# Kernel tuning notes

Measured on AMD Instinct MI355X. Metric: run time of the kernel, lower is better.

The kernel has to match this reference:

```python
import jax, jax.numpy as jnp
import numpy as np

N, K, D, L = 50000, 32, 128, 64
NEG_SLOPE = 0.2


def setup_inputs() -> dict:
    key = jax.random.key(0)
    k1, k2, k3, k4 = jax.random.split(key, 4)
    para_neighbors = jax.random.normal(k1, (N, K, D), dtype=jnp.float32)
    para_nei_labels = jax.random.uniform(k2, (N, K, L), dtype=jnp.float32)
    # glorot-uniform-style params
    lim_lin = float(np.sqrt(6.0 / (D + D)))
    linear = jax.random.uniform(k3, (D, D), minval=-lim_lin, maxval=lim_lin, dtype=jnp.float32)
    lim_e = float(np.sqrt(6.0 / (D + 1)))
    e_vec = jax.random.uniform(k4, (D, 1), minval=-lim_e, maxval=lim_e, dtype=jnp.float32)
    bias = jnp.zeros((K, 1), dtype=jnp.float32)
    return {"para_neighbors": para_neighbors, "para_nei_labels": para_nei_labels,
            "linear": linear, "e_vec": e_vec, "bias": bias}


def reference(para_neighbors, para_nei_labels, linear, e_vec, bias):
    # [N, K, D] @ [D, D] -> [N, K, D], LeakyReLU(0.2)
    h = jax.nn.leaky_relu(jnp.einsum('nkd,de->nke', para_neighbors, linear), NEG_SLOPE)
    # attention logits: [N, K, 1] + bias [K, 1] -> LeakyReLU
    e = jax.nn.leaky_relu(jnp.einsum('nkd,do->nko', h, e_vec) + bias, NEG_SLOPE)
    # softmax over neighbor axis (axis=1)
    alpha = jax.nn.softmax(e, axis=1)[..., 0]  # [N, K]
    # weighted label aggregation: [N, K] x [N, K, L] -> [N, L]
    pred_labels = jnp.einsum('nk,nkl->nl', alpha, para_nei_labels)
    return pred_labels
```

## Files before the change

kernel.cpp:

```cpp
#include <hip/hip_runtime.h>
#include <hip/hip_bf16.h>

#define NN 50000
#define KK 32
#define DD 128
#define LL 64
#define NEG 0.2f

typedef __bf16 bf16x8 __attribute__((ext_vector_type(8)));
typedef unsigned short u16x8 __attribute__((ext_vector_type(8)));
typedef float f32x4 __attribute__((ext_vector_type(4)));

__device__ __forceinline__ unsigned short f2bf(float f) {
    unsigned u = __builtin_bit_cast(unsigned, f);
    unsigned r = (u + 0x7fffu + ((u >> 16) & 1u)) >> 16;
    return (unsigned short)r;
}

__device__ __forceinline__ bf16x8 pack_bf16x8(float4 a, float4 b) {
    bf16x8 t;
    t[0] = (__bf16)a.x; t[1] = (__bf16)a.y; t[2] = (__bf16)a.z; t[3] = (__bf16)a.w;
    t[4] = (__bf16)b.x; t[5] = (__bf16)b.y; t[6] = (__bf16)b.z; t[7] = (__bf16)b.w;
    return t;
}


__global__ void prep_w_kernel(const float* __restrict__ lin,
                              unsigned short* __restrict__ wimg) {
    int idx = blockIdx.x * blockDim.x + threadIdx.x;
    if (idx >= DD * DD) return;
    int d = idx >> 7;
    int e = idx & 127;
    unsigned b = (unsigned)e * 256u + (unsigned)d * 2u;
    b ^= ((unsigned)(e & 7)) << 4;
    wimg[b >> 1] = f2bf(lin[idx]);
}

__global__ __launch_bounds__(256)
void attn_fused_kernel(const float* __restrict__ X,
                       const float* __restrict__ LAB,
                       const unsigned short* __restrict__ WIMG,
                       const float* __restrict__ EV,
                       const float* __restrict__ BIAS,
                       float* __restrict__ OUT)
{
    __shared__ __align__(16) unsigned short w_lds[DD * DD];
    __shared__ float alpha_lds[4 * 64];

    const int tid  = threadIdx.x;
    const int wave = tid >> 6;
    const int lane = tid & 63;
    const int lo16 = lane & 15;
    const int g    = lane >> 4;

    {
        const float4* wsrc = reinterpret_cast<const float4*>(WIMG);
        float4* wdst = reinterpret_cast<float4*>(w_lds);
        #pragma unroll
        for (int i = 0; i < 8; ++i)
            wdst[i * 256 + tid] = wsrc[i * 256 + tid];
    }

    float evr[8];
    #pragma unroll
    for (int ct = 0; ct < 8; ++ct) evr[ct] = EV[ct * 16 + lo16];

    float biasr[2][4];
    #pragma unroll
    for (int h = 0; h < 2; ++h)
        #pragma unroll
        for (int r = 0; r < 4; ++r)
            biasr[h][r] = BIAS[h * 16 + g * 4 + r];

    const long rowbase = (long)blockIdx.x * 256 + wave * 64;
    bf16x8 a[4][4];
    #pragma unroll
    for (int mt = 0; mt < 4; ++mt) {
        const float* xr = X + (rowbase + mt * 16 + lo16) * (long)DD;
        #pragma unroll
        for (int kt = 0; kt < 4; ++kt) {
            const float4* p = reinterpret_cast<const float4*>(xr + kt * 32 + g * 8);
            float4 u0 = p[0];
            float4 u1 = p[1];
            a[mt][kt] = pack_bf16x8(u0, u1);
        }
    }

    __syncthreads();

    float pe[4][4];
    #pragma unroll
    for (int mt = 0; mt < 4; ++mt)
        #pragma unroll
        for (int r = 0; r < 4; ++r) pe[mt][r] = 0.f;

    const char* wl = reinterpret_cast<const char*>(w_lds);
    #pragma unroll
    for (int ct = 0; ct < 8; ++ct) {
        bf16x8 b[4];
        const int n = ct * 16 + lo16;
        #pragma unroll
        for (int kt = 0; kt < 4; ++kt) {
            unsigned off = (unsigned)(n * 256 + kt * 64 + g * 16);
            off ^= ((unsigned)(n & 7)) << 4;
            b[kt] = *reinterpret_cast<const bf16x8*>(wl + off);
        }
        f32x4 acc[4];
        #pragma unroll
        for (int mt = 0; mt < 4; ++mt) { acc[mt][0]=0.f; acc[mt][1]=0.f; acc[mt][2]=0.f; acc[mt][3]=0.f; }
        #pragma unroll
        for (int kt = 0; kt < 4; ++kt)
            #pragma unroll
            for (int mt = 0; mt < 4; ++mt)
                acc[mt] = __builtin_amdgcn_mfma_f32_16x16x32_bf16(a[mt][kt], b[kt], acc[mt], 0, 0, 0);
        #pragma unroll
        for (int mt = 0; mt < 4; ++mt)
            #pragma unroll
            for (int r = 0; r < 4; ++r) {
                float h = acc[mt][r];
                h = (h > 0.f) ? h : NEG * h;
                pe[mt][r] += h * evr[ct];
            }
    }

    #pragma unroll
    for (int mt = 0; mt < 4; ++mt)
        #pragma unroll
        for (int r = 0; r < 4; ++r) {
            float v = pe[mt][r];
            v += __shfl_xor(v, 1);
            v += __shfl_xor(v, 2);
            v += __shfl_xor(v, 4);
            v += __shfl_xor(v, 8);
            v += biasr[mt & 1][r];
            pe[mt][r] = (v > 0.f) ? v : NEG * v;
        }

    #pragma unroll
    for (int h = 0; h < 2; ++h) {
        float m = -3.4e38f;
        #pragma unroll
        for (int t = 0; t < 2; ++t)
            #pragma unroll
            for (int r = 0; r < 4; ++r) m = fmaxf(m, pe[2 * h + t][r]);
        m = fmaxf(m, __shfl_xor(m, 16));
        m = fmaxf(m, __shfl_xor(m, 32));
        float p[2][4];
        float s = 0.f;
        #pragma unroll
        for (int t = 0; t < 2; ++t)
            #pragma unroll
            for (int r = 0; r < 4; ++r) {
                p[t][r] = __expf(pe[2 * h + t][r] - m);
                s += p[t][r];
            }
        s += __shfl_xor(s, 16);
        s += __shfl_xor(s, 32);
        float inv = 1.f / s;
        if (lo16 == 0) {
            #pragma unroll
            for (int t = 0; t < 2; ++t)
                #pragma unroll
                for (int r = 0; r < 4; ++r)
                    alpha_lds[wave * 64 + h * 32 + t * 16 + g * 4 + r] = p[t][r] * inv;
        }
    }

    __syncthreads();

    const int c2 = (lane & 31) * 2;
    const int kh = lane >> 5;
    #pragma unroll
    for (int h = 0; h < 2; ++h) {
        const long n = (long)blockIdx.x * 8 + wave * 2 + h;
        const float* lab = LAB + n * (long)(KK * LL) + kh * 16 * LL + c2;
        float ax = 0.f, ay = 0.f;
        #pragma unroll
        for (int k = 0; k < 16; ++k) {
            float al = alpha_lds[wave * 64 + h * 32 + kh * 16 + k];
            float2 lv = *reinterpret_cast<const float2*>(lab + k * LL);
            ax += al * lv.x;
            ay += al * lv.y;
        }
        ax += __shfl_xor(ax, 32);
        ay += __shfl_xor(ay, 32);
        if (lane < 32) {
            float2 o;
            o.x = ax; o.y = ay;
            *reinterpret_cast<float2*>(OUT + n * LL + c2) = o;
        }
    }
}

extern "C" void kernel_launch(void* const* d_in, const int* in_sizes, int n_in,
                              void* d_out, int out_size, void* d_ws, size_t ws_size,
                              hipStream_t stream) {
    const float* X    = (const float*)d_in[0];
    const float* LAB  = (const float*)d_in[1];
    const float* LIN  = (const float*)d_in[2];
    const float* EV   = (const float*)d_in[3];
    const float* BIAS = (const float*)d_in[4];
    float* OUT = (float*)d_out;
    unsigned short* wimg = (unsigned short*)d_ws;

    prep_w_kernel<<<64, 256, 0, stream>>>(LIN, wimg);
    attn_fused_kernel<<<NN / 8, 256, 0, stream>>>(X, LAB, wimg, EV, BIAS, OUT);
}
```

Before: 225.1 us.

## Split fused kernel into alpha computation and label aggregation kernels

Splits the single fused kernel in two. The first kernel computes the attention weights and writes them into the output buffer as scratch, 32 floats per row. The second kernel reads those weights back, broadcasts them across lanes with shuffles and aggregates the labels. The aim is to decouple the MFMA-heavy stage from the bandwidth-bound label read so each kernel can keep more loads in flight. The cost is an extra launch, a global round-trip for alpha, and losing the overlap between the two stages inside one block.

```diff
diff --git a/kernel.cpp b/kernel.cpp
--- a/kernel.cpp
+++ b/kernel.cpp
@@ -8,7 +8,6 @@
 #define NEG 0.2f
 
 typedef __bf16 bf16x8 __attribute__((ext_vector_type(8)));
-typedef unsigned short u16x8 __attribute__((ext_vector_type(8)));
 typedef float f32x4 __attribute__((ext_vector_type(4)));
 
 __device__ __forceinline__ unsigned short f2bf(float f) {
@@ -37,15 +36,13 @@
 }
 
 __global__ __launch_bounds__(256)
-void attn_fused_kernel(const float* __restrict__ X,
-                       const float* __restrict__ LAB,
+void attn_alpha_kernel(const float* __restrict__ X,
                        const unsigned short* __restrict__ WIMG,
                        const float* __restrict__ EV,
                        const float* __restrict__ BIAS,
                        float* __restrict__ OUT)
 {
     __shared__ __align__(16) unsigned short w_lds[DD * DD];
-    __shared__ float alpha_lds[4 * 64];
 
     const int tid  = threadIdx.x;
     const int wave = tid >> 6;
@@ -67,10 +64,10 @@
 
     float biasr[2][4];
     #pragma unroll
-    for (int h = 0; h < 2; ++h)
+    for (int t = 0; t < 2; ++t)
         #pragma unroll
         for (int r = 0; r < 4; ++r)
-            biasr[h][r] = BIAS[h * 16 + g * 4 + r];
+            biasr[t][r] = BIAS[t * 16 + g * 4 + r];
 
     const long rowbase = (long)blockIdx.x * 256 + wave * 64;
     bf16x8 a[4][4];
@@ -158,38 +155,43 @@
         s += __shfl_xor(s, 32);
         float inv = 1.f / s;
         if (lo16 == 0) {
-            #pragma unroll
-            for (int t = 0; t < 2; ++t)
-                #pragma unroll
-                for (int r = 0; r < 4; ++r)
-                    alpha_lds[wave * 64 + h * 32 + t * 16 + g * 4 + r] = p[t][r] * inv;
-        }
-    }
-
-    __syncthreads();
-
-    const int c2 = (lane & 31) * 2;
-    const int kh = lane >> 5;
-    #pragma unroll
-    for (int h = 0; h < 2; ++h) {
-        const long n = (long)blockIdx.x * 8 + wave * 2 + h;
-        const float* lab = LAB + n * (long)(KK * LL) + kh * 16 * LL + c2;
-        float ax = 0.f, ay = 0.f;
-        #pragma unroll
-        for (int k = 0; k < 16; ++k) {
-            float al = alpha_lds[wave * 64 + h * 32 + kh * 16 + k];
-            float2 lv = *reinterpret_cast<const float2*>(lab + k * LL);
-            ax += al * lv.x;
-            ay += al * lv.y;
-        }
-        ax += __shfl_xor(ax, 32);
-        ay += __shfl_xor(ay, 32);
-        if (lane < 32) {
-            float2 o;
-            o.x = ax; o.y = ay;
-            *reinterpret_cast<float2*>(OUT + n * LL + c2) = o;
-        }
-    }
+            const long n = (long)blockIdx.x * 8 + wave * 2 + h;
+            #pragma unroll
+            for (int t = 0; t < 2; ++t) {
+                f32x4 av;
+                av[0] = p[t][0] * inv; av[1] = p[t][1] * inv;
+                av[2] = p[t][2] * inv; av[3] = p[t][3] * inv;
+                *reinterpret_cast<f32x4*>(OUT + n * LL + t * 16 + g * 4) = av;
+            }
+        }
+    }
+}
+
+__global__ __launch_bounds__(256)
+void label_agg_kernel(const float* __restrict__ LAB,
+                      float* __restrict__ OUT)
+{
+    const int tid  = threadIdx.x;
+    const int wave = tid >> 6;
+    const int lane = tid & 63;
+    const int l32  = lane & 31;
+    const int half = lane >> 5;
+
+    const long n = (long)blockIdx.x * 8 + wave * 2 + half;
+
+    const float al = OUT[n * LL + l32];
+
+    const float* lab = LAB + n * (long)(KK * LL) + l32 * 2;
+    float ax = 0.f, ay = 0.f;
+    #pragma unroll
+    for (int k = 0; k < KK; ++k) {
+        float a = __shfl(al, k, 32);
+        float2 lv = *reinterpret_cast<const float2*>(lab + k * LL);
+        ax += a * lv.x;
+        ay += a * lv.y;
+    }
+    float2 o; o.x = ax; o.y = ay;
+    *reinterpret_cast<float2*>(OUT + n * LL + l32 * 2) = o;
 }
 
 extern "C" void kernel_launch(void* const* d_in, const int* in_sizes, int n_in,
@@ -204,5 +206,6 @@
     unsigned short* wimg = (unsigned short*)d_ws;
 
     prep_w_kernel<<<64, 256, 0, stream>>>(LIN, wimg);
-    attn_fused_kernel<<<NN / 8, 256, 0, stream>>>(X, LAB, wimg, EV, BIAS, OUT);
-}
+    attn_alpha_kernel<<<NN / 8, 256, 0, stream>>>(X, wimg, EV, BIAS, OUT);
+    label_agg_kernel<<<NN / 8, 256, 0, stream>>>(LAB, OUT);
+}
```

Result: slower. 234.0 us (+3.9%).
